# Kernel tuning notes

Measured on AMD Instinct MI355X. Metric: run time of the kernel, lower is better.

## Reference

```python
import jax, jax.numpy as jnp
import numpy as np

B = 16384
F_IN = 768
F_OUT = 512

def setup_inputs() -> dict:
    key = jax.random.key(0)
    k1, k2, k3, k4, k5, k6 = jax.random.split(key, 6)
    # densified sparse multi-hot boards (post to_dense())
    stm = jax.random.uniform(k1, (B, F_IN), dtype=jnp.float32)
    nstm = jax.random.uniform(k2, (B, F_IN), dtype=jnp.float32)
    s1 = 1.0 / np.sqrt(F_IN)
    s2 = 1.0 / np.sqrt(2 * F_OUT)
    W1 = jax.random.normal(k3, (F_OUT, F_IN), dtype=jnp.float32) * s1
    b1 = jax.random.normal(k4, (F_OUT,), dtype=jnp.float32) * s1
    W2 = jax.random.normal(k5, (1, 2 * F_OUT), dtype=jnp.float32) * s2
    b2 = jax.random.normal(k6, (1,), dtype=jnp.float32) * s2
    return {"stm": stm, "nstm": nstm, "W1": W1, "b1": b1, "W2": W2, "b2": b2}

def reference(stm, nstm, W1, b1, W2, b2):
    # shared feature transformer applied to both perspectives
    stm_p = stm @ W1.T + b1    # [B, F_OUT]
    nstm_p = nstm @ W1.T + b1  # [B, F_OUT]
    hidden = jnp.clip(jnp.concatenate((stm_p, nstm_p), axis=1), 0.0, 1.0)  # [B, 2*F_OUT]
    return jax.nn.sigmoid(hidden @ W2.T + b2)  # [B, 1]
```

## Files before the change

kernel.cpp:

```cpp
#include <hip/hip_runtime.h>
#include <hip/hip_bf16.h>

#define BATCH 16384
#define FIN   768
#define FOUT  512

#define BK 32
#define NT (FIN / BK)
#define BM 128
#define BN 256

typedef __attribute__((ext_vector_type(8))) short short8;
typedef __attribute__((ext_vector_type(4))) float floatx4;

__device__ __forceinline__ unsigned int cvt_pk_bf16(float a, float b) {
    unsigned int r;
    asm("v_cvt_pk_bf16_f32 %0, %1, %2" : "=v"(r) : "v"(a), "v"(b));
    return r;
}

__device__ __forceinline__ void load_lds_16(const void* g, void* l) {
    __builtin_amdgcn_global_load_lds(
        (const __attribute__((address_space(1))) unsigned int*)g,
        (__attribute__((address_space(3))) unsigned int*)l,
        16, 0, 0);
}

__global__ __launch_bounds__(256) void cvt_w1(
    const float* __restrict__ W1, unsigned short* __restrict__ W1b)
{
    int base = (blockIdx.x * 256 + threadIdx.x) * 8;
    float4 a = *(const float4*)(W1 + base);
    float4 b = *(const float4*)(W1 + base + 4);
    uint4 o;
    o.x = cvt_pk_bf16(a.x, a.y); o.y = cvt_pk_bf16(a.z, a.w);
    o.z = cvt_pk_bf16(b.x, b.y); o.w = cvt_pk_bf16(b.z, b.w);
    *(uint4*)(W1b + base) = o;
}

__global__ __launch_bounds__(1024, 4) void pn_gemm(
    const float* __restrict__ stm, const float* __restrict__ nstm,
    const unsigned short* __restrict__ W1b, const float* __restrict__ b1,
    const float* __restrict__ W2, float* __restrict__ P)
{
    __shared__ __align__(16) unsigned short As[2][256 * 32];
    __shared__ __align__(16) unsigned short Bs[2][256 * 32];

    const int tid  = threadIdx.x;
    const int lane = tid & 63;
    const int wave = tid >> 6;
    const int wr   = wave >> 2;
    const int wc   = wave & 3;
    const int quad = lane >> 4;
    const int l16  = lane & 15;
    const int l3   = l16 & 3;

    const int bm    = blockIdx.x >> 1;
    const int n_idx = blockIdx.x & 1;
    const int b0    = bm * BM;
    const int n0    = n_idx * BN;

    const int arow = tid >> 2;
    const int ach  = tid & 3;
    const float* aSrc =
        ((arow < BM) ? stm  + (size_t)(b0 + arow) * FIN
                     : nstm + (size_t)(b0 + arow - BM) * FIN) + ach * 8;
    const int aOff = arow * 32 + (ach ^ (arow & 3)) * 8;

    const int brow = lane >> 2;
    const int bch  = (lane & 3) ^ (brow & 3);
    const unsigned short* bSrc =
        W1b + (size_t)(n0 + wave * 16 + brow) * FIN + bch * 8;

    floatx4 acc[4][4];
    #pragma unroll
    for (int i = 0; i < 4; ++i)
        #pragma unroll
        for (int j = 0; j < 4; ++j)
            acc[i][j] = (floatx4)0.0f;

    float4 ap0 = *(const float4*)(aSrc);
    float4 ap1 = *(const float4*)(aSrc + 4);
    load_lds_16(bSrc, &Bs[0][wave * 512]);

    for (int t = 0; t < NT; ++t) {
        const int cur = t & 1;
        const int nxt = cur ^ 1;

        {
            uint4 o;
            o.x = cvt_pk_bf16(ap0.x, ap0.y); o.y = cvt_pk_bf16(ap0.z, ap0.w);
            o.z = cvt_pk_bf16(ap1.x, ap1.y); o.w = cvt_pk_bf16(ap1.z, ap1.w);
            *(uint4*)(&As[cur][aOff]) = o;
        }
        __syncthreads();

        if (t + 1 < NT) {
            const int kn = (t + 1) * BK;
            load_lds_16(bSrc + kn, &Bs[nxt][wave * 512]);
            ap0 = *(const float4*)(aSrc + kn);
            ap1 = *(const float4*)(aSrc + kn + 4);
        }

        short8 af[4], bfr[4];
        #pragma unroll
        for (int mi = 0; mi < 4; ++mi) {
            const int m = wr * 64 + mi * 16 + l16;
            af[mi] = *(const short8*)(&As[cur][m * 32 + ((quad ^ l3) * 8)]);
        }
        #pragma unroll
        for (int ni = 0; ni < 4; ++ni) {
            const int n = wc * 64 + ni * 16 + l16;
            bfr[ni] = *(const short8*)(&Bs[cur][n * 32 + ((quad ^ l3) * 8)]);
        }
        #pragma unroll
        for (int mi = 0; mi < 4; ++mi)
            #pragma unroll
            for (int ni = 0; ni < 4; ++ni)
                acc[mi][ni] = __builtin_amdgcn_mfma_f32_16x16x32_bf16(
                    af[mi], bfr[ni], acc[mi][ni], 0, 0, 0);
    }

    float b1v[4], w2v[4];
    const float* w2base = (wr < 2) ? W2 : W2 + FOUT;
    #pragma unroll
    for (int ni = 0; ni < 4; ++ni) {
        int col = n0 + wc * 64 + ni * 16 + l16;
        b1v[ni] = b1[col];
        w2v[ni] = w2base[col];
    }

    __syncthreads();
    float* Epi = (float*)As;

    #pragma unroll
    for (int mi = 0; mi < 4; ++mi) {
        #pragma unroll
        for (int r = 0; r < 4; ++r) {
            float s = 0.0f;
            #pragma unroll
            for (int ni = 0; ni < 4; ++ni) {
                float h = acc[mi][ni][r] + b1v[ni];
                h = fminf(fmaxf(h, 0.0f), 1.0f);
                s += h * w2v[ni];
            }
            s += __shfl_xor(s, 1);
            s += __shfl_xor(s, 2);
            s += __shfl_xor(s, 4);
            s += __shfl_xor(s, 8);
            if (l16 == 0) {
                Epi[(wr * 64 + mi * 16 + quad * 4 + r) * 4 + wc] = s;
            }
        }
    }
    __syncthreads();

    if (tid < BM) {
        float x = 0.0f;
        #pragma unroll
        for (int j = 0; j < 4; ++j)
            x += Epi[tid * 4 + j] + Epi[(tid + BM) * 4 + j];
        P[n_idx * BATCH + b0 + tid] = x;
    }
}

__global__ __launch_bounds__(256) void finish(
    const float* __restrict__ P, const float* __restrict__ b2,
    float* __restrict__ out)
{
    int i = blockIdx.x * 256 + threadIdx.x;
    float x = b2[0] + P[i] + P[BATCH + i];
    out[i] = 1.0f / (1.0f + expf(-x));
}

extern "C" void kernel_launch(void* const* d_in, const int* in_sizes, int n_in,
                              void* d_out, int out_size, void* d_ws, size_t ws_size,
                              hipStream_t stream)
{
    (void)in_sizes; (void)n_in; (void)out_size; (void)ws_size;
    const float* stm  = (const float*)d_in[0];
    const float* nstm = (const float*)d_in[1];
    const float* W1   = (const float*)d_in[2];
    const float* b1   = (const float*)d_in[3];
    const float* W2   = (const float*)d_in[4];
    const float* b2   = (const float*)d_in[5];
    float* out = (float*)d_out;
    unsigned short* W1b = (unsigned short*)d_ws;
    float* P = (float*)((char*)d_ws + FOUT * FIN * 2);

    cvt_w1<<<dim3((FOUT * FIN) / (256 * 8)), dim3(256), 0, stream>>>(W1, W1b);
    pn_gemm<<<dim3((BATCH / BM) * 2), dim3(1024), 0, stream>>>(
        stm, nstm, W1b, b1, W2, P);
    finish<<<dim3(BATCH / 256), dim3(256), 0, stream>>>(P, b2, out);
}
```

Baseline: 154.3 us.

## Stream fp32 A tiles directly to LDS with triple-buffered async pipeline

Loads the fp32 activation tiles straight into LDS with global_load_lds instead of through registers, converting to bf16 when fragments are read. Deepens buffering to three stages with prefetch two tiles ahead and explicit vmcnt-based barriers so global loads stay in flight across iterations. Also remaps block ids so neighboring blocks share tiles. This raises LDS usage substantially and doubles LDS read bytes for A, which may limit occupancy or add LDS bandwidth pressure.

```diff
diff --git a/kernel.cpp b/kernel.cpp
--- a/kernel.cpp
+++ b/kernel.cpp
@@ -25,6 +25,19 @@
         (__attribute__((address_space(3))) unsigned int*)l,
         16, 0, 0);
 }
+
+#define BAR_VM3() do {                                               \
+    __builtin_amdgcn_sched_barrier(0);                               \
+    asm volatile("s_waitcnt vmcnt(3) lgkmcnt(0)" ::: "memory");      \
+    __builtin_amdgcn_s_barrier();                                    \
+    __builtin_amdgcn_sched_barrier(0);                               \
+} while (0)
+#define BAR_VM0() do {                                               \
+    __builtin_amdgcn_sched_barrier(0);                               \
+    asm volatile("s_waitcnt vmcnt(0) lgkmcnt(0)" ::: "memory");      \
+    __builtin_amdgcn_s_barrier();                                    \
+    __builtin_amdgcn_sched_barrier(0);                               \
+} while (0)
 
 __global__ __launch_bounds__(256) void cvt_w1(
     const float* __restrict__ W1, unsigned short* __restrict__ W1b)
@@ -43,8 +56,8 @@
     const unsigned short* __restrict__ W1b, const float* __restrict__ b1,
     const float* __restrict__ W2, float* __restrict__ P)
 {
-    __shared__ __align__(16) unsigned short As[2][256 * 32];
-    __shared__ __align__(16) unsigned short Bs[2][256 * 32];
+    __shared__ __align__(16) float          Asf[3][256 * 32];
+    __shared__ __align__(16) unsigned short Bs[3][256 * 32];
 
     const int tid  = threadIdx.x;
     const int lane = tid & 63;
@@ -53,19 +66,25 @@
     const int wc   = wave & 3;
     const int quad = lane >> 4;
     const int l16  = lane & 15;
-    const int l3   = l16 & 3;
-
-    const int bm    = blockIdx.x >> 1;
-    const int n_idx = blockIdx.x & 1;
+
+    const int sbid  = (blockIdx.x & 7) * 32 + (blockIdx.x >> 3);
+    const int bm    = sbid >> 1;
+    const int n_idx = sbid & 1;
     const int b0    = bm * BM;
     const int n0    = n_idx * BN;
 
-    const int arow = tid >> 2;
-    const int ach  = tid & 3;
-    const float* aSrc =
-        ((arow < BM) ? stm  + (size_t)(b0 + arow) * FIN
-                     : nstm + (size_t)(b0 + arow - BM) * FIN) + ach * 8;
-    const int aOff = arow * 32 + (ach ^ (arow & 3)) * 8;
+    const int aRowIn = (lane >> 3);
+    const int aChunk = (lane & 7) ^ aRowIn;
+    const int arow0  = (wave * 2 + 0) * 8 + aRowIn;
+    const int arow1  = (wave * 2 + 1) * 8 + aRowIn;
+    const float* aSrc0 =
+        ((arow0 < BM) ? stm  + (size_t)(b0 + arow0) * FIN
+                      : nstm + (size_t)(b0 + arow0 - BM) * FIN) + aChunk * 4;
+    const float* aSrc1 =
+        ((arow1 < BM) ? stm  + (size_t)(b0 + arow1) * FIN
+                      : nstm + (size_t)(b0 + arow1 - BM) * FIN) + aChunk * 4;
+    const int aDst0 = (wave * 2 + 0) * 256;
+    const int aDst1 = (wave * 2 + 1) * 256;
 
     const int brow = lane >> 2;
     const int bch  = (lane & 3) ^ (brow & 3);
@@ -79,39 +98,41 @@
         for (int j = 0; j < 4; ++j)
             acc[i][j] = (floatx4)0.0f;
 
-    float4 ap0 = *(const float4*)(aSrc);
-    float4 ap1 = *(const float4*)(aSrc + 4);
-    load_lds_16(bSrc, &Bs[0][wave * 512]);
-
+    load_lds_16(aSrc0,      &Asf[0][aDst0]);
+    load_lds_16(aSrc1,      &Asf[0][aDst1]);
+    load_lds_16(bSrc,       &Bs[0][wave * 512]);
+    load_lds_16(aSrc0 + BK, &Asf[1][aDst0]);
+    load_lds_16(aSrc1 + BK, &Asf[1][aDst1]);
+    load_lds_16(bSrc + BK,  &Bs[1][wave * 512]);
+
+    int bc = 0;
     for (int t = 0; t < NT; ++t) {
-        const int cur = t & 1;
-        const int nxt = cur ^ 1;
-
-        {
-            uint4 o;
-            o.x = cvt_pk_bf16(ap0.x, ap0.y); o.y = cvt_pk_bf16(ap0.z, ap0.w);
-            o.z = cvt_pk_bf16(ap1.x, ap1.y); o.w = cvt_pk_bf16(ap1.z, ap1.w);
-            *(uint4*)(&As[cur][aOff]) = o;
-        }
-        __syncthreads();
-
-        if (t + 1 < NT) {
-            const int kn = (t + 1) * BK;
-            load_lds_16(bSrc + kn, &Bs[nxt][wave * 512]);
-            ap0 = *(const float4*)(aSrc + kn);
-            ap1 = *(const float4*)(aSrc + kn + 4);
+        if (t + 1 < NT) { BAR_VM3(); } else { BAR_VM0(); }
+
+        if (t + 2 < NT) {
+            int bp = bc + 2; if (bp >= 3) bp -= 3;
+            const int kn = (t + 2) * BK;
+            load_lds_16(aSrc0 + kn, &Asf[bp][aDst0]);
+            load_lds_16(aSrc1 + kn, &Asf[bp][aDst1]);
+            load_lds_16(bSrc + kn,  &Bs[bp][wave * 512]);
         }
 
         short8 af[4], bfr[4];
         #pragma unroll
         for (int mi = 0; mi < 4; ++mi) {
             const int m = wr * 64 + mi * 16 + l16;
-            af[mi] = *(const short8*)(&As[cur][m * 32 + ((quad ^ l3) * 8)]);
+            const float* ar = &Asf[bc][m * 32];
+            float4 lo = *(const float4*)(ar + (((2 * quad    ) ^ (l16 & 7)) << 2));
+            float4 hi = *(const float4*)(ar + (((2 * quad + 1) ^ (l16 & 7)) << 2));
+            uint4 o;
+            o.x = cvt_pk_bf16(lo.x, lo.y); o.y = cvt_pk_bf16(lo.z, lo.w);
+            o.z = cvt_pk_bf16(hi.x, hi.y); o.w = cvt_pk_bf16(hi.z, hi.w);
+            af[mi] = *(short8*)&o;
         }
         #pragma unroll
         for (int ni = 0; ni < 4; ++ni) {
             const int n = wc * 64 + ni * 16 + l16;
-            bfr[ni] = *(const short8*)(&Bs[cur][n * 32 + ((quad ^ l3) * 8)]);
+            bfr[ni] = *(const short8*)(&Bs[bc][n * 32 + ((quad ^ (n & 3)) * 8)]);
         }
         #pragma unroll
         for (int mi = 0; mi < 4; ++mi)
@@ -119,6 +140,8 @@
             for (int ni = 0; ni < 4; ++ni)
                 acc[mi][ni] = __builtin_amdgcn_mfma_f32_16x16x32_bf16(
                     af[mi], bfr[ni], acc[mi][ni], 0, 0, 0);
+
+        bc = (bc == 2) ? 0 : bc + 1;
     }
 
     float b1v[4], w2v[4];
@@ -131,7 +154,7 @@
     }
 
     __syncthreads();
-    float* Epi = (float*)As;
+    float* Epi = (float*)Asf;
 
     #pragma unroll
     for (int mi = 0; mi < 4; ++mi) {
```

New measurement: 160.6 us. 1.04x slower.

## Load activations straight to registers and triple-buffer W1 tiles in LDS

Applied to the files above, without the earlier changes.

Activation tiles are now loaded from global memory straight into registers and converted to bf16 there, so they no longer pass through LDS. Only the W1 tiles are staged, through a triple-buffered LDS ring with K depth 64, prefetched two steps ahead with one barrier per iteration. The wave layout changes from 2x4 to 8x2, so each wave covers 32 rows by 128 columns, and block IDs are remapped for locality across XCDs. The aim is fewer LDS writes and barriers and better latency hiding. In exchange, each A row is read by two waves from global, and correctness relies on implicit vmcnt waits for the async LDS loads.

```diff
diff --git a/kernel.cpp b/kernel.cpp
--- a/kernel.cpp
+++ b/kernel.cpp
@@ -5,7 +5,7 @@
 #define FIN   768
 #define FOUT  512
 
-#define BK 32
+#define BK 64
 #define NT (FIN / BK)
 #define BM 128
 #define BN 256
@@ -43,103 +43,135 @@
     const unsigned short* __restrict__ W1b, const float* __restrict__ b1,
     const float* __restrict__ W2, float* __restrict__ P)
 {
-    __shared__ __align__(16) unsigned short As[2][256 * 32];
-    __shared__ __align__(16) unsigned short Bs[2][256 * 32];
+    __shared__ __align__(16) unsigned short Bs[3][256 * 64];
 
     const int tid  = threadIdx.x;
     const int lane = tid & 63;
     const int wave = tid >> 6;
-    const int wr   = wave >> 2;
-    const int wc   = wave & 3;
+    const int wr   = wave >> 1;
+    const int wc   = wave & 1;
     const int quad = lane >> 4;
     const int l16  = lane & 15;
-    const int l3   = l16 & 3;
-
-    const int bm    = blockIdx.x >> 1;
-    const int n_idx = blockIdx.x & 1;
+
+    const int sbid  = (blockIdx.x & 7) * 32 + (blockIdx.x >> 3);
+    const int bm    = sbid >> 1;
+    const int n_idx = sbid & 1;
     const int b0    = bm * BM;
     const int n0    = n_idx * BN;
 
-    const int arow = tid >> 2;
-    const int ach  = tid & 3;
-    const float* aSrc =
-        ((arow < BM) ? stm  + (size_t)(b0 + arow) * FIN
-                     : nstm + (size_t)(b0 + arow - BM) * FIN) + ach * 8;
-    const int aOff = arow * 32 + (ach ^ (arow & 3)) * 8;
-
-    const int brow = lane >> 2;
-    const int bch  = (lane & 3) ^ (brow & 3);
-    const unsigned short* bSrc =
-        W1b + (size_t)(n0 + wave * 16 + brow) * FIN + bch * 8;
-
-    floatx4 acc[4][4];
+    const float* aPtr0;
+    const float* aPtr1;
+    {
+        int m0 = wr * 32 + 0 * 16 + l16;
+        int m1 = wr * 32 + 1 * 16 + l16;
+        aPtr0 = ((m0 < BM) ? stm + (size_t)(b0 + m0) * FIN
+                           : nstm + (size_t)(b0 + m0 - BM) * FIN) + quad * 8;
+        aPtr1 = ((m1 < BM) ? stm + (size_t)(b0 + m1) * FIN
+                           : nstm + (size_t)(b0 + m1 - BM) * FIN) + quad * 8;
+    }
+
+    const int brow = lane >> 3;
+    const int bch  = (lane & 7) ^ brow;
+    const unsigned short* bSrc0 =
+        W1b + (size_t)(n0 + (wave * 2 + 0) * 8 + brow) * FIN + bch * 8;
+    const unsigned short* bSrc1 =
+        W1b + (size_t)(n0 + (wave * 2 + 1) * 8 + brow) * FIN + bch * 8;
+    const int bDst0 = (wave * 2 + 0) * 512;
+    const int bDst1 = (wave * 2 + 1) * 512;
+
+    floatx4 acc[2][8];
     #pragma unroll
-    for (int i = 0; i < 4; ++i)
+    for (int i = 0; i < 2; ++i)
         #pragma unroll
-        for (int j = 0; j < 4; ++j)
+        for (int j = 0; j < 8; ++j)
             acc[i][j] = (floatx4)0.0f;
 
-    float4 ap0 = *(const float4*)(aSrc);
-    float4 ap1 = *(const float4*)(aSrc + 4);
-    load_lds_16(bSrc, &Bs[0][wave * 512]);
-
+    load_lds_16(bSrc0,      &Bs[0][bDst0]);
+    load_lds_16(bSrc1,      &Bs[0][bDst1]);
+    load_lds_16(bSrc0 + BK, &Bs[1][bDst0]);
+    load_lds_16(bSrc1 + BK, &Bs[1][bDst1]);
+    __builtin_amdgcn_sched_barrier(0);
+    asm volatile("s_waitcnt vmcnt(2) lgkmcnt(0)" ::: "memory");
+    __builtin_amdgcn_s_barrier();
+    __builtin_amdgcn_sched_barrier(0);
+
+    int bc = 0;
     for (int t = 0; t < NT; ++t) {
-        const int cur = t & 1;
-        const int nxt = cur ^ 1;
-
-        {
-            uint4 o;
-            o.x = cvt_pk_bf16(ap0.x, ap0.y); o.y = cvt_pk_bf16(ap0.z, ap0.w);
-            o.z = cvt_pk_bf16(ap1.x, ap1.y); o.w = cvt_pk_bf16(ap1.z, ap1.w);
-            *(uint4*)(&As[cur][aOff]) = o;
+        if (t + 2 < NT) {
+            int bp = bc + 2; if (bp >= 3) bp -= 3;
+            const int kn2 = (t + 2) * BK;
+            load_lds_16(bSrc0 + kn2, &Bs[bp][bDst0]);
+            load_lds_16(bSrc1 + kn2, &Bs[bp][bDst1]);
         }
-        __syncthreads();
-
-        if (t + 1 < NT) {
-            const int kn = (t + 1) * BK;
-            load_lds_16(bSrc + kn, &Bs[nxt][wave * 512]);
-            ap0 = *(const float4*)(aSrc + kn);
-            ap1 = *(const float4*)(aSrc + kn + 4);
+
+        #pragma unroll
+        for (int kk = 0; kk < 2; ++kk) {
+            const int koff = t * BK + kk * 32;
+            const int c    = kk * 4 + quad;
+
+            short8 af0, af1;
+            {
+                float4 lo = *(const float4*)(aPtr0 + koff);
+                float4 hi = *(const float4*)(aPtr0 + koff + 4);
+                uint4 o;
+                o.x = cvt_pk_bf16(lo.x, lo.y); o.y = cvt_pk_bf16(lo.z, lo.w);
+                o.z = cvt_pk_bf16(hi.x, hi.y); o.w = cvt_pk_bf16(hi.z, hi.w);
+                af0 = *(short8*)&o;
+            }
+            {
+                float4 lo = *(const float4*)(aPtr1 + koff);
+                float4 hi = *(const float4*)(aPtr1 + koff + 4);
+                uint4 o;
+                o.x = cvt_pk_bf16(lo.x, lo.y); o.y = cvt_pk_bf16(lo.z, lo.w);
+                o.z = cvt_pk_bf16(hi.x, hi.y); o.w = cvt_pk_bf16(hi.z, hi.w);
+                af1 = *(short8*)&o;
+            }
+
+            #pragma unroll
+            for (int nh = 0; nh < 2; ++nh) {
+                short8 bfr[4];
+                #pragma unroll
+                for (int j = 0; j < 4; ++j) {
+                    const int n = wc * 128 + (nh * 4 + j) * 16 + l16;
+                    bfr[j] = *(const short8*)(
+                        &Bs[bc][n * 64 + ((c ^ (n & 7)) * 8)]);
+                }
+                #pragma unroll
+                for (int j = 0; j < 4; ++j) {
+                    acc[0][nh * 4 + j] = __builtin_amdgcn_mfma_f32_16x16x32_bf16(
+                        af0, bfr[j], acc[0][nh * 4 + j], 0, 0, 0);
+                    acc[1][nh * 4 + j] = __builtin_amdgcn_mfma_f32_16x16x32_bf16(
+                        af1, bfr[j], acc[1][nh * 4 + j], 0, 0, 0);
+                }
+            }
         }
 
-        short8 af[4], bfr[4];
-        #pragma unroll
-        for (int mi = 0; mi < 4; ++mi) {
-            const int m = wr * 64 + mi * 16 + l16;
-            af[mi] = *(const short8*)(&As[cur][m * 32 + ((quad ^ l3) * 8)]);
-        }
-        #pragma unroll
-        for (int ni = 0; ni < 4; ++ni) {
-            const int n = wc * 64 + ni * 16 + l16;
-            bfr[ni] = *(const short8*)(&Bs[cur][n * 32 + ((quad ^ l3) * 8)]);
-        }
-        #pragma unroll
-        for (int mi = 0; mi < 4; ++mi)
-            #pragma unroll
-            for (int ni = 0; ni < 4; ++ni)
-                acc[mi][ni] = __builtin_amdgcn_mfma_f32_16x16x32_bf16(
-                    af[mi], bfr[ni], acc[mi][ni], 0, 0, 0);
-    }
-
-    float b1v[4], w2v[4];
-    const float* w2base = (wr < 2) ? W2 : W2 + FOUT;
+        bc = (bc == 2) ? 0 : bc + 1;
+
+        __builtin_amdgcn_sched_barrier(0);
+        asm volatile("s_waitcnt lgkmcnt(0)" ::: "memory");
+        __builtin_amdgcn_s_barrier();
+        __builtin_amdgcn_sched_barrier(0);
+    }
+
+    float b1v[8], w2v[8];
+    const float* w2base = (wr < 4) ? W2 : W2 + FOUT;
     #pragma unroll
-    for (int ni = 0; ni < 4; ++ni) {
-        int col = n0 + wc * 64 + ni * 16 + l16;
+    for (int ni = 0; ni < 8; ++ni) {
+        int col = n0 + wc * 128 + ni * 16 + l16;
         b1v[ni] = b1[col];
         w2v[ni] = w2base[col];
     }
 
-    __syncthreads();
-    float* Epi = (float*)As;
+    float* Epi = (float*)Bs;
 
     #pragma unroll
-    for (int mi = 0; mi < 4; ++mi) {
+    for (int mi = 0; mi < 2; ++mi) {
         #pragma unroll
         for (int r = 0; r < 4; ++r) {
             float s = 0.0f;
             #pragma unroll
-            for (int ni = 0; ni < 4; ++ni) {
+            for (int ni = 0; ni < 8; ++ni) {
                 float h = acc[mi][ni][r] + b1v[ni];
                 h = fminf(fmaxf(h, 0.0f), 1.0f);
                 s += h * w2v[ni];
@@ -149,17 +181,15 @@
             s += __shfl_xor(s, 4);
             s += __shfl_xor(s, 8);
             if (l16 == 0) {
-                Epi[(wr * 64 + mi * 16 + quad * 4 + r) * 4 + wc] = s;
+                Epi[(wr * 32 + mi * 16 + quad * 4 + r) * 2 + wc] = s;
             }
         }
     }
     __syncthreads();
 
     if (tid < BM) {
-        float x = 0.0f;
-        #pragma unroll
-        for (int j = 0; j < 4; ++j)
-            x += Epi[tid * 4 + j] + Epi[(tid + BM) * 4 + j];
+        float x = Epi[tid * 2] + Epi[tid * 2 + 1]
+                + Epi[(tid + BM) * 2] + Epi[(tid + BM) * 2 + 1];
         P[n_idx * BATCH + b0 + tid] = x;
     }
 }
```

Measured after the change: 167.0 us. 1.08x slower.
